# Kernel optimization log

Hardware: AMD Instinct MI355X
Metric: run time of the kernel (lower is better)

Reference implementation:

```python
import jax, jax.numpy as jnp
import numpy as np

B, N, C, H, K = 16, 1024, 384, 6, 8
HID = int(C * 2.0)  # mlp_ratio = 2.0
HD = C // H


def _layernorm(x, w, b, eps=1e-5):
    m = x.mean(-1, keepdims=True)
    v = ((x - m) ** 2).mean(-1, keepdims=True)
    return (x - m) * jax.lax.rsqrt(v + eps) * w + b


def setup_inputs() -> dict:
    key = jax.random.key(0)
    ks = jax.random.split(key, 16)
    x = jax.random.normal(ks[0], (B, N, C), jnp.float32)
    # knn indices within each batch, offset by batch*N (as in get_knn_index)
    idx = jax.random.randint(ks[1], (B, K, N), 0, N)
    base = jnp.arange(B, dtype=jnp.int32)[:, None, None] * N
    knn_index = (idx + base).reshape(-1).astype(jnp.int32)
    s = 0.02
    p = {
        "x": x,
        "knn_index": knn_index,
        "ln1_w": jnp.ones((C,), jnp.float32),
        "ln1_b": jnp.zeros((C,), jnp.float32),
        "w_qkv": jax.random.normal(ks[2], (C, 3 * C), jnp.float32) * s,  # qkv_bias=False
        "w_proj": jax.random.normal(ks[3], (C, C), jnp.float32) * s,
        "b_proj": jnp.zeros((C,), jnp.float32),
        "w_knn": jax.random.normal(ks[4], (2 * C, C), jnp.float32) * s,
        "b_knn": jnp.zeros((C,), jnp.float32),
        "w_merge": jax.random.normal(ks[5], (2 * C, C), jnp.float32) * s,
        "b_merge": jnp.zeros((C,), jnp.float32),
        "ln2_w": jnp.ones((C,), jnp.float32),
        "ln2_b": jnp.zeros((C,), jnp.float32),
        "w_fc1": jax.random.normal(ks[6], (C, HID), jnp.float32) * s,
        "b_fc1": jnp.zeros((HID,), jnp.float32),
        "w_fc2": jax.random.normal(ks[7], (HID, C), jnp.float32) * s,
        "b_fc2": jnp.zeros((C,), jnp.float32),
    }
    return p


def reference(x, knn_index, ln1_w, ln1_b, w_qkv, w_proj, b_proj, w_knn, b_knn,
              w_merge, b_merge, ln2_w, ln2_b, w_fc1, b_fc1, w_fc2, b_fc2):
    nx = _layernorm(x, ln1_w, ln1_b)  # [B,N,C]

    # --- self attention ---
    qkv = (nx @ w_qkv).reshape(B, N, 3, H, HD)
    q, k, v = qkv[:, :, 0], qkv[:, :, 1], qkv[:, :, 2]  # [B,N,H,HD]
    scale = HD ** (-0.5)
    attn = jnp.einsum("bnhd,bmhd->bhnm", q, k) * scale
    attn = jax.nn.softmax(attn, axis=-1)
    a_out = jnp.einsum("bhnm,bmhd->bnhd", attn, v).reshape(B, N, C)
    x1 = a_out @ w_proj + b_proj

    # --- graph feature: gather, relative concat, Linear+LeakyReLU, max over k ---
    feat = nx.reshape(B * N, C)[knn_index].reshape(B, K, N, C)
    center = nx[:, None, :, :]  # [B,1,N,C]
    g = jnp.concatenate([feat - center, jnp.broadcast_to(center, (B, K, N, C))], axis=-1)
    knn_f = jax.nn.leaky_relu(g @ w_knn + b_knn, negative_slope=0.2)
    knn_f = knn_f.max(axis=1)  # [B,N,C]

    x1 = jnp.concatenate([x1, knn_f], axis=-1) @ w_merge + b_merge
    x = x + x1

    # --- MLP ---
    h = _layernorm(x, ln2_w, ln2_b)
    h = jax.nn.gelu(h @ w_fc1 + b_fc1, approximate=False) @ w_fc2 + b_fc2
    return x + h
```

## Files before the change

### kernel.cpp

```cpp
#include <hip/hip_runtime.h>
#include <hip/hip_bf16.h>
#include <math.h>

#define BN_ROWS 16384
#define CDIM 384
#define NH 6
#define BBATCH 16
#define NNN 1024

typedef unsigned short u16;
typedef unsigned int u32;
typedef __attribute__((ext_vector_type(8))) short short8;
typedef __attribute__((ext_vector_type(4))) float floatx4;

__device__ __forceinline__ float b2f(u16 s) { return __uint_as_float(((u32)s) << 16); }
__device__ __forceinline__ u16 f2b(float f) {
    __hip_bfloat16 h = __float2bfloat16(f);
    u16 s; __builtin_memcpy(&s, &h, 2); return s;
}
__device__ __forceinline__ u32 cvt_pk_bf16(float lo, float hi) {
    u32 r;
    asm("v_cvt_pk_bf16_f32 %0, %1, %2" : "=v"(r) : "v"(lo), "v"(hi));
    return r;
}
__device__ __forceinline__ void gload_lds16(const u16* g, u16* l) {
    __builtin_amdgcn_global_load_lds(
        (const __attribute__((address_space(1))) unsigned int*)g,
        (__attribute__((address_space(3))) unsigned int*)l, 16, 0, 0);
}

__global__ __launch_bounds__(256) void pack_all(
    const float* __restrict__ W0, u16* __restrict__ T0,
    const float* __restrict__ W1, u16* __restrict__ T1,
    const float* __restrict__ W2, u16* __restrict__ T2,
    const float* __restrict__ W3, u16* __restrict__ T3,
    const float* __restrict__ W4, u16* __restrict__ T4,
    const float* __restrict__ W5, u16* __restrict__ T5)
{
    const float* W; u16* T; int K, N;
    switch (blockIdx.z) {
        case 0: W = W0; T = T0; K = 384; N = 1152; break;
        case 1: W = W1; T = T1; K = 384; N = 384;  break;
        case 2: W = W2; T = T2; K = 768; N = 384;  break;
        case 3: W = W3; T = T3; K = 768; N = 384;  break;
        case 4: W = W4; T = T4; K = 384; N = 768;  break;
        default: W = W5; T = T5; K = 768; N = 384; break;
    }
    const int n0 = blockIdx.x * 32, k0 = blockIdx.y * 32;
    if (n0 >= N || k0 >= K) return;
    __shared__ float s[32][33];
    const int tx = threadIdx.x & 31, ty = threadIdx.x >> 5;
#pragma unroll
    for (int i = 0; i < 4; ++i)
        s[ty + 8 * i][tx] = W[(size_t)(k0 + ty + 8 * i) * N + n0 + tx];
    __syncthreads();
#pragma unroll
    for (int i = 0; i < 4; ++i)
        T[(size_t)(n0 + ty + 8 * i) * K + k0 + tx] = f2b(s[tx][ty + 8 * i]);
}

__global__ __launch_bounds__(64) void ln_kernel(const float* __restrict__ xin,
                                                const float* __restrict__ w,
                                                const float* __restrict__ b,
                                                u16* __restrict__ out)
{
    const int row = blockIdx.x;
    const int t = threadIdx.x;
    const size_t base = (size_t)row * CDIM;
    float v[6];
#pragma unroll
    for (int i = 0; i < 6; ++i) v[i] = xin[base + t + 64 * i];
    float s = 0.f, s2 = 0.f;
#pragma unroll
    for (int i = 0; i < 6; ++i) { s += v[i]; s2 += v[i] * v[i]; }
#pragma unroll
    for (int m = 1; m < 64; m <<= 1) {
        s  += __shfl_xor(s,  m, 64);
        s2 += __shfl_xor(s2, m, 64);
    }
    const float mean = s * (1.0f / CDIM);
    const float var  = s2 * (1.0f / CDIM) - mean * mean;
    const float rs   = rsqrtf(var + 1e-5f);
#pragma unroll
    for (int i = 0; i < 6; ++i) {
        int c = t + 64 * i;
        out[base + c] = f2b((v[i] - mean) * rs * w[c] + b[c]);
    }
}

template<int ACT, bool HAS_BIAS, bool HAS_RES, bool OUT_F32, int MODE, int NT, bool SWZ>
__global__ __launch_bounds__(256) void gemm_mfma_kernel(
    const u16* __restrict__ A, int lda,
    const u16* __restrict__ Bt, const u16* __restrict__ Bt2, int ldbt,
    u16* Cb, u16* Cb2, float* Cf, int ldc,
    const float* __restrict__ bias,
    const float* res,
    int K)
{
    constexpr int NTL = NT / 32;
    __shared__ u16 As[2][128 * 32];
    __shared__ u16 Bs[2][NT * 32];
    const int tid  = threadIdx.x;
    const int wv   = tid >> 6;
    const int lane = tid & 63;
    const int l15  = lane & 15;
    const int quad = lane >> 4;

    int m0, n0;
    if (SWZ) {
        const int nbx = gridDim.x;
        const int total = nbx * gridDim.y;
        int lin = blockIdx.x + nbx * blockIdx.y;
        const int cpx = total >> 3;
        lin = (lin & 7) * cpx + (lin >> 3);
        m0 = (lin / nbx) * 128;
        n0 = (lin % nbx) * NT;
    } else {
        m0 = blockIdx.y * 128;
        n0 = blockIdx.x * NT;
    }

    const int woffm = (wv >> 1) * 64;
    const int woffn = (wv & 1) * (NT / 2);

    const u16* bsrc = (MODE == 2 && n0 >= 384) ? Bt2 : Bt;
    const int  bn0  = (MODE == 2 && n0 >= 384) ? (n0 - 384) : n0;

    floatx4 acc[4][NTL];
#pragma unroll
    for (int mt = 0; mt < 4; ++mt)
#pragma unroll
        for (int nt = 0; nt < NTL; ++nt) acc[mt][nt] = (floatx4){0.f, 0.f, 0.f, 0.f};

    const int gsw  = 8 * ((lane & 3) ^ ((lane >> 3) & 3));
    const int rloc = lane >> 2;
    const int rdsw = 8 * (quad ^ ((l15 >> 1) & 3));

    auto stage = [&](int kt, int p) {
#pragma unroll
        for (int j = 0; j < 2; ++j) {
            const int slab = 32 * wv + 16 * j;
            gload_lds16(A + (size_t)(m0 + slab + rloc) * lda + kt + gsw, &As[p][slab * 32]);
        }
        if (NT == 128) {
#pragma unroll
            for (int j = 0; j < 2; ++j) {
                const int slab = 32 * wv + 16 * j;
                gload_lds16(bsrc + (size_t)(bn0 + slab + rloc) * ldbt + kt + gsw, &Bs[p][slab * 32]);
            }
        } else {
            const int slab = 16 * wv;
            gload_lds16(bsrc + (size_t)(bn0 + slab + rloc) * ldbt + kt + gsw, &Bs[p][slab * 32]);
        }
    };

    stage(0, 0);
    stage(32, 1);
    int cur = 0;
    for (int kt = 0; kt < K; kt += 32) {
        if (kt + 32 < K) {
            if constexpr (NT == 128) asm volatile("s_waitcnt vmcnt(4)" ::: "memory");
            else                     asm volatile("s_waitcnt vmcnt(3)" ::: "memory");
        } else {
            asm volatile("s_waitcnt vmcnt(0)" ::: "memory");
        }
        __builtin_amdgcn_sched_barrier(0);
        __builtin_amdgcn_s_barrier();
        __builtin_amdgcn_sched_barrier(0);

        short8 af[4], bf[NTL];
#pragma unroll
        for (int mt = 0; mt < 4; ++mt)
            af[mt] = *(const short8*)(As[cur] + (woffm + mt * 16 + l15) * 32 + rdsw);
#pragma unroll
        for (int nt = 0; nt < NTL; ++nt)
            bf[nt] = *(const short8*)(Bs[cur] + (woffn + nt * 16 + l15) * 32 + rdsw);
#pragma unroll
        for (int mt = 0; mt < 4; ++mt)
#pragma unroll
            for (int nt = 0; nt < NTL; ++nt)
                acc[mt][nt] = __builtin_amdgcn_mfma_f32_16x16x32_bf16(
                    bf[nt], af[mt], acc[mt][nt], 0, 0, 0);
        __builtin_amdgcn_sched_barrier(0);
        __builtin_amdgcn_s_barrier();
        __builtin_amdgcn_sched_barrier(0);
        if (kt + 64 < K) stage(kt + 64, cur);
        cur ^= 1;
    }

#pragma unroll
    for (int mt = 0; mt < 4; ++mt) {
        const int gr = m0 + woffm + mt * 16 + l15;
#pragma unroll
        for (int nt = 0; nt < NTL; ++nt) {
            const int gc0 = n0 + woffn + nt * 16 + quad * 4;
            float v4[4];
#pragma unroll
            for (int rr = 0; rr < 4; ++rr) v4[rr] = acc[mt][nt][rr];
            if (HAS_BIAS) {
                const floatx4 bv = *(const floatx4*)(bias + gc0);
#pragma unroll
                for (int rr = 0; rr < 4; ++rr) v4[rr] += bv[rr];
            }
            if (MODE == 2) {
                if (gc0 >= 384) {
                    const floatx4 bv = *(const floatx4*)(bias + gc0 - 384);
#pragma unroll
                    for (int rr = 0; rr < 4; ++rr) v4[rr] += bv[rr];
                }
            }
            if (ACT == 1) {
#pragma unroll
                for (int rr = 0; rr < 4; ++rr)
                    v4[rr] = 0.5f * v4[rr] * (1.0f + erff(v4[rr] * 0.70710678118654752f));
            }
            if (HAS_RES) {
                const floatx4 rv = *(const floatx4*)(res + (size_t)gr * ldc + gc0);
#pragma unroll
                for (int rr = 0; rr < 4; ++rr) v4[rr] += rv[rr];
            }
            if (MODE == 1) {
                const int t3  = gc0 / 384;
                const int rem = gc0 - t3 * 384;
                const int hh = rem >> 6, dd = rem & 63;
                const int bb = gr >> 10, nn = gr & 1023;
                u32 lo = cvt_pk_bf16(v4[0], v4[1]);
                u32 hi = cvt_pk_bf16(v4[2], v4[3]);
                *(uint2*)(Cb + ((size_t)((bb * 6 + hh) * 1024 + nn)) * 192 + t3 * 64 + dd) =
                    make_uint2(lo, hi);
            } else if (MODE == 2) {
                u32 lo = cvt_pk_bf16(v4[0], v4[1]);
                u32 hi = cvt_pk_bf16(v4[2], v4[3]);
                if (gc0 < 384)
                    *(uint2*)(Cb  + (size_t)gr * 384 + gc0)       = make_uint2(lo, hi);
                else
                    *(uint2*)(Cb2 + (size_t)gr * 384 + gc0 - 384) = make_uint2(lo, hi);
            } else if (OUT_F32) {
                floatx4 vv = {v4[0], v4[1], v4[2], v4[3]};
                *(floatx4*)(Cf + (size_t)gr * ldc + gc0) = vv;
            } else {
                u32 lo = cvt_pk_bf16(v4[0], v4[1]);
                u32 hi = cvt_pk_bf16(v4[2], v4[3]);
                *(uint2*)(Cb + (size_t)gr * ldc + gc0) = make_uint2(lo, hi);
            }
        }
    }
}

__global__ __launch_bounds__(256) void attn_mfma_kernel(const u16* __restrict__ qkv2,
                                                        u16* __restrict__ aout)
{
    const int id = blockIdx.x;
    const int rxcd = id & 7;
    const int j = id >> 3;
    const int slab = rxcd + 8 * (j % 12);
    const int qtile = j / 12;
    const int b = slab / NH, h = slab % NH;

    const int wave = threadIdx.x >> 6;
    const int lane = threadIdx.x & 63;
    const int l15 = lane & 15;
    const int quad = lane >> 4;
    const int qbase = qtile * 128 + wave * 32;
    const int tid = threadIdx.x;

    const u16* slabp = qkv2 + ((size_t)(b * NH + h) << 10) * 192;

    __shared__ __align__(16) u16 Ks[64 * 72];
    __shared__ __align__(16) u16 Vt[64 * 72];
    __shared__ __align__(16) u16 Ps[4][32 * 72];
    __shared__ __align__(16) float Ls[4][32];

    short8 qf[2][2];
#pragma unroll
    for (int nt = 0; nt < 2; ++nt) {
        const u16* qrow = slabp + (size_t)(qbase + nt * 16 + l15) * 192;
        qf[nt][0] = *(const short8*)(qrow + quad * 8);
        qf[nt][1] = *(const short8*)(qrow + 32 + quad * 8);
    }

    float rowsum[2] = {0.f, 0.f};
    floatx4 Oacc[2][4];
#pragma unroll
    for (int mt = 0; mt < 2; ++mt)
#pragma unroll
        for (int nt = 0; nt < 4; ++nt) Oacc[mt][nt] = (floatx4){0.f, 0.f, 0.f, 0.f};

    const int key = tid >> 2, dblk = (tid & 3) * 16;
    const int kp2 = tid & 31, db = (tid >> 5) * 8;
    uint4 kr0, kr1, vr0, vr1;
    {
        const u16* kp = slabp + (size_t)key * 192 + 64 + dblk;
        kr0 = *(const uint4*)(kp);
        kr1 = *(const uint4*)(kp + 8);
        const u16* vp = slabp + (size_t)(2 * kp2) * 192 + 128 + db;
        vr0 = *(const uint4*)(vp);
        vr1 = *(const uint4*)(vp + 192);
    }

    for (int kc = 0; kc < NNN; kc += 64) {
        *(uint4*)(Ks + key * 72 + dblk)     = kr0;
        *(uint4*)(Ks + key * 72 + dblk + 8) = kr1;
        {
            u32 a0[4] = {vr0.x, vr0.y, vr0.z, vr0.w};
            u32 a1[4] = {vr1.x, vr1.y, vr1.z, vr1.w};
#pragma unroll
            for (int i = 0; i < 4; ++i) {
                u32 lo = __builtin_amdgcn_perm(a1[i], a0[i], 0x05040100u);
                u32 hi = __builtin_amdgcn_perm(a1[i], a0[i], 0x07060302u);
                *(u32*)(Vt + (size_t)(db + 2 * i)     * 72 + 2 * kp2) = lo;
                *(u32*)(Vt + (size_t)(db + 2 * i + 1) * 72 + 2 * kp2) = hi;
            }
        }
        __syncthreads();

        if (kc + 64 < NNN) {
            const u16* kp = slabp + (size_t)(kc + 64 + key) * 192 + 64 + dblk;
            kr0 = *(const uint4*)(kp);
            kr1 = *(const uint4*)(kp + 8);
            const u16* vp = slabp + (size_t)(kc + 64 + 2 * kp2) * 192 + 128 + db;
            vr0 = *(const uint4*)(vp);
            vr1 = *(const uint4*)(vp + 192);
        }

        floatx4 sc[4][2];
        __builtin_amdgcn_s_setprio(1);
#pragma unroll
        for (int kt_ = 0; kt_ < 4; ++kt_) {
            short8 kf0 = *(const short8*)(Ks + (kt_ * 16 + l15) * 72 + quad * 8);
            short8 kf1 = *(const short8*)(Ks + (kt_ * 16 + l15) * 72 + 32 + quad * 8);
#pragma unroll
            for (int nt = 0; nt < 2; ++nt) {
                floatx4 s = {0.f, 0.f, 0.f, 0.f};
                s = __builtin_amdgcn_mfma_f32_16x16x32_bf16(kf0, qf[nt][0], s, 0, 0, 0);
                s = __builtin_amdgcn_mfma_f32_16x16x32_bf16(kf1, qf[nt][1], s, 0, 0, 0);
                sc[kt_][nt] = s;
            }
        }
        __builtin_amdgcn_s_setprio(0);

#pragma unroll
        for (int kt_ = 0; kt_ < 4; ++kt_)
#pragma unroll
            for (int nt = 0; nt < 2; ++nt) {
                float pv[4];
#pragma unroll
                for (int rr = 0; rr < 4; ++rr) {
                    pv[rr] = __expf(sc[kt_][nt][rr] * 0.125f);
                    rowsum[nt] += pv[rr];
                }
                u32 lo = cvt_pk_bf16(pv[0], pv[1]);
                u32 hi = cvt_pk_bf16(pv[2], pv[3]);
                *(uint2*)(Ps[wave] + (nt * 16 + l15) * 72 + kt_ * 16 + quad * 4) =
                    make_uint2(lo, hi);
            }

        short8 pf[2][2];
#pragma unroll
        for (int mt = 0; mt < 2; ++mt) {
            pf[mt][0] = *(const short8*)(Ps[wave] + (mt * 16 + l15) * 72 + quad * 8);
            pf[mt][1] = *(const short8*)(Ps[wave] + (mt * 16 + l15) * 72 + 32 + quad * 8);
        }
        __builtin_amdgcn_s_setprio(1);
#pragma unroll
        for (int nt = 0; nt < 4; ++nt) {
#pragma unroll
            for (int kk = 0; kk < 2; ++kk) {
                short8 vf = *(const short8*)(Vt + (size_t)(nt * 16 + l15) * 72 + kk * 32 + quad * 8);
#pragma unroll
                for (int mt = 0; mt < 2; ++mt)
                    Oacc[mt][nt] = __builtin_amdgcn_mfma_f32_16x16x32_bf16(
                        pf[mt][kk], vf, Oacc[mt][nt], 0, 0, 0);
            }
        }
        __builtin_amdgcn_s_setprio(0);
        __syncthreads();
    }

#pragma unroll
    for (int nt = 0; nt < 2; ++nt) {
        float l = rowsum[nt];
        l += __shfl_xor(l, 16, 64);
        l += __shfl_xor(l, 32, 64);
        if (quad == 0) Ls[wave][nt * 16 + l15] = l;
    }
#pragma unroll
    for (int mt = 0; mt < 2; ++mt) {
        float4 lv = *(const float4*)&Ls[wave][mt * 16 + quad * 4];
        float li[4] = {lv.x, lv.y, lv.z, lv.w};
#pragma unroll
        for (int rr = 0; rr < 4; ++rr) {
            float inv = 1.0f / li[rr];
            int q = qbase + mt * 16 + quad * 4 + rr;
#pragma unroll
            for (int nt = 0; nt < 4; ++nt)
                aout[(size_t)(b * NNN + q) * CDIM + h * 64 + nt * 16 + l15] =
                    f2b(Oacc[mt][nt][rr] * inv);
        }
    }
}

__global__ __launch_bounds__(128) void knnmax_kernel(const u16* __restrict__ t1,
                                                     const u16* __restrict__ t2,
                                                     const int* __restrict__ idx,
                                                     u16* __restrict__ x1cat)
{
    const int bn = blockIdx.x * 2 + (threadIdx.x >> 6);
    const int lane = threadIdx.x & 63;
    if (lane >= 48) return;
    const int b = bn >> 10, n = bn & 1023;
    int ind[8];
#pragma unroll
    for (int k = 0; k < 8; ++k) ind[k] = idx[b * 8192 + k * 1024 + n];
    const int c0 = lane * 8;
    const size_t rbase = (size_t)bn * CDIM + c0;
    short8 v1 = *(const short8*)(t1 + rbase);
    short8 v2 = *(const short8*)(t2 + rbase);
    float basef[8], mx[8];
#pragma unroll
    for (int j = 0; j < 8; ++j) {
        basef[j] = b2f((u16)v2[j]) - b2f((u16)v1[j]);
        mx[j] = -1e30f;
    }
#pragma unroll
    for (int k = 0; k < 8; ++k) {
        short8 nv = *(const short8*)(t1 + (size_t)ind[k] * CDIM + c0);
#pragma unroll
        for (int j = 0; j < 8; ++j) {
            float v = b2f((u16)nv[j]) + basef[j];
            v = (v > 0.f) ? v : 0.2f * v;
            mx[j] = fmaxf(mx[j], v);
        }
    }
    short8 ov;
#pragma unroll
    for (int j = 0; j < 8; ++j) ov[j] = (short)f2b(mx[j]);
    *(short8*)(x1cat + (size_t)bn * 768 + CDIM + c0) = ov;
}

extern "C" void kernel_launch(void* const* d_in, const int* in_sizes, int n_in,
                              void* d_out, int out_size, void* d_ws, size_t ws_size,
                              hipStream_t stream)
{
    (void)in_sizes; (void)n_in; (void)out_size; (void)ws_size;
    const float* x     = (const float*)d_in[0];
    const int*   knn   = (const int*)d_in[1];
    const float* ln1w  = (const float*)d_in[2];
    const float* ln1b  = (const float*)d_in[3];
    const float* wqkv  = (const float*)d_in[4];
    const float* wproj = (const float*)d_in[5];
    const float* bproj = (const float*)d_in[6];
    const float* wknn  = (const float*)d_in[7];
    const float* bknn  = (const float*)d_in[8];
    const float* wmrg  = (const float*)d_in[9];
    const float* bmrg  = (const float*)d_in[10];
    const float* ln2w  = (const float*)d_in[11];
    const float* ln2b  = (const float*)d_in[12];
    const float* wfc1  = (const float*)d_in[13];
    const float* bfc1  = (const float*)d_in[14];
    const float* wfc2  = (const float*)d_in[15];
    const float* bfc2  = (const float*)d_in[16];

    u16* wsb = (u16*)d_ws;
    const size_t RE = (size_t)BN_ROWS * CDIM;
    u16* nxb   = wsb;
    u16* qkvb  = wsb + RE;
    u16* x1cat = wsb + RE;
    u16* t1b   = wsb + 3 * RE;
    u16* hinb  = wsb;
    u16* h1b   = wsb + RE;
    u16* wqkvT  = wsb + 4 * RE;
    u16* wprojT = wqkvT + 442368;
    u16* wknnT  = wprojT + 147456;
    u16* wmrgT  = wknnT + 294912;
    u16* wfc1T  = wmrgT + 294912;
    u16* wfc2T  = wfc1T + 294912;
    u16*   aoutb = (u16*)d_out;
    u16*   t2b   = (u16*)d_out;
    float* xmid  = (float*)d_out;

    pack_all<<<dim3(36, 24, 6), 256, 0, stream>>>(
        wqkv, wqkvT, wproj, wprojT, wknn, wknnT, wmrg, wmrgT, wfc1, wfc1T, wfc2, wfc2T);
    ln_kernel<<<BN_ROWS, 64, 0, stream>>>(x, ln1w, ln1b, nxb);
    gemm_mfma_kernel<0, false, false, false, 1, 128, true><<<dim3(9, 128), 256, 0, stream>>>(
        nxb, CDIM, wqkvT, nullptr, CDIM, qkvb, nullptr, nullptr, 0, nullptr, nullptr, CDIM);
    attn_mfma_kernel<<<768, 256, 0, stream>>>(qkvb, aoutb);
    gemm_mfma_kernel<0, true, false, false, 0, 64, true><<<dim3(6, 128), 256, 0, stream>>>(
        aoutb, CDIM, wprojT, nullptr, CDIM, x1cat, nullptr, nullptr, 768, bproj, nullptr, CDIM);
    gemm_mfma_kernel<0, false, false, false, 2, 128, true><<<dim3(6, 128), 256, 0, stream>>>(
        nxb, CDIM, wknnT, wknnT + 384, 768, t1b, t2b, nullptr, CDIM, bknn, nullptr, CDIM);
    knnmax_kernel<<<BN_ROWS / 2, 128, 0, stream>>>(t1b, t2b, knn, x1cat);
    gemm_mfma_kernel<0, true, true, true, 0, 64, true><<<dim3(6, 128), 256, 0, stream>>>(
        x1cat, 768, wmrgT, nullptr, 768, nullptr, nullptr, xmid, CDIM, bmrg, x, 768);
    ln_kernel<<<BN_ROWS, 64, 0, stream>>>(xmid, ln2w, ln2b, hinb);
    gemm_mfma_kernel<1, true, false, false, 0, 128, true><<<dim3(6, 128), 256, 0, stream>>>(
        hinb, CDIM, wfc1T, nullptr, CDIM, h1b, nullptr, nullptr, 768, bfc1, nullptr, CDIM);
    gemm_mfma_kernel<0, true, true, true, 0, 64, true><<<dim3(6, 128), 256, 0, stream>>>(
        h1b, 768, wfc2T, nullptr, 768, nullptr, nullptr, (float*)d_out, CDIM, bfc2, xmid, 768);
}
```

Baseline: 309.2 us.

## Shrink GEMM tiles to 64x64 with simpler double-buffered pipeline

```diff
diff --git a/kernel.cpp b/kernel.cpp
--- a/kernel.cpp
+++ b/kernel.cpp
@@ -88,8 +88,8 @@
     }
 }
 
-template<int ACT, bool HAS_BIAS, bool HAS_RES, bool OUT_F32, int MODE, int NT, bool SWZ>
-__global__ __launch_bounds__(256) void gemm_mfma_kernel(
+template<int ACT, bool HAS_BIAS, bool HAS_RES, bool OUT_F32, int MODE, bool SWZ>
+__global__ __launch_bounds__(256, 6) void gemm_mfma_kernel(
     const u16* __restrict__ A, int lda,
     const u16* __restrict__ Bt, const u16* __restrict__ Bt2, int ldbt,
     u16* Cb, u16* Cb2, float* Cf, int ldc,
@@ -97,9 +97,8 @@
     const float* res,
     int K)
 {
-    constexpr int NTL = NT / 32;
-    __shared__ u16 As[2][128 * 32];
-    __shared__ u16 Bs[2][NT * 32];
+    __shared__ u16 As[2][64 * 32];
+    __shared__ u16 Bs[2][64 * 32];
     const int tid  = threadIdx.x;
     const int wv   = tid >> 6;
     const int lane = tid & 63;
@@ -113,86 +112,63 @@
         int lin = blockIdx.x + nbx * blockIdx.y;
         const int cpx = total >> 3;
         lin = (lin & 7) * cpx + (lin >> 3);
-        m0 = (lin / nbx) * 128;
-        n0 = (lin % nbx) * NT;
+        m0 = (lin / nbx) * 64;
+        n0 = (lin % nbx) * 64;
     } else {
-        m0 = blockIdx.y * 128;
-        n0 = blockIdx.x * NT;
-    }
-
-    const int woffm = (wv >> 1) * 64;
-    const int woffn = (wv & 1) * (NT / 2);
+        m0 = blockIdx.y * 64;
+        n0 = blockIdx.x * 64;
+    }
+
+    const int woffm = (wv >> 1) * 32;
+    const int woffn = (wv & 1) * 32;
 
     const u16* bsrc = (MODE == 2 && n0 >= 384) ? Bt2 : Bt;
     const int  bn0  = (MODE == 2 && n0 >= 384) ? (n0 - 384) : n0;
 
-    floatx4 acc[4][NTL];
-#pragma unroll
-    for (int mt = 0; mt < 4; ++mt)
-#pragma unroll
-        for (int nt = 0; nt < NTL; ++nt) acc[mt][nt] = (floatx4){0.f, 0.f, 0.f, 0.f};
+    floatx4 acc[2][2];
+#pragma unroll
+    for (int mt = 0; mt < 2; ++mt)
+#pragma unroll
+        for (int nt = 0; nt < 2; ++nt) acc[mt][nt] = (floatx4){0.f, 0.f, 0.f, 0.f};
 
     const int gsw  = 8 * ((lane & 3) ^ ((lane >> 3) & 3));
     const int rloc = lane >> 2;
     const int rdsw = 8 * (quad ^ ((l15 >> 1) & 3));
 
     auto stage = [&](int kt, int p) {
-#pragma unroll
-        for (int j = 0; j < 2; ++j) {
-            const int slab = 32 * wv + 16 * j;
-            gload_lds16(A + (size_t)(m0 + slab + rloc) * lda + kt + gsw, &As[p][slab * 32]);
-        }
-        if (NT == 128) {
-#pragma unroll
-            for (int j = 0; j < 2; ++j) {
-                const int slab = 32 * wv + 16 * j;
-                gload_lds16(bsrc + (size_t)(bn0 + slab + rloc) * ldbt + kt + gsw, &Bs[p][slab * 32]);
-            }
-        } else {
-            const int slab = 16 * wv;
-            gload_lds16(bsrc + (size_t)(bn0 + slab + rloc) * ldbt + kt + gsw, &Bs[p][slab * 32]);
-        }
+        const int slab = 16 * wv;
+        gload_lds16(A    + (size_t)(m0  + slab + rloc) * lda  + kt + gsw, &As[p][slab * 32]);
+        gload_lds16(bsrc + (size_t)(bn0 + slab + rloc) * ldbt + kt + gsw, &Bs[p][slab * 32]);
     };
 
     stage(0, 0);
-    stage(32, 1);
+    __syncthreads();
     int cur = 0;
     for (int kt = 0; kt < K; kt += 32) {
-        if (kt + 32 < K) {
-            if constexpr (NT == 128) asm volatile("s_waitcnt vmcnt(4)" ::: "memory");
-            else                     asm volatile("s_waitcnt vmcnt(3)" ::: "memory");
-        } else {
-            asm volatile("s_waitcnt vmcnt(0)" ::: "memory");
-        }
-        __builtin_amdgcn_sched_barrier(0);
-        __builtin_amdgcn_s_barrier();
-        __builtin_amdgcn_sched_barrier(0);
-
-        short8 af[4], bf[NTL];
-#pragma unroll
-        for (int mt = 0; mt < 4; ++mt)
+        if (kt + 32 < K) stage(kt + 32, cur ^ 1);
+
+        short8 af[2], bf[2];
+#pragma unroll
+        for (int mt = 0; mt < 2; ++mt)
             af[mt] = *(const short8*)(As[cur] + (woffm + mt * 16 + l15) * 32 + rdsw);
 #pragma unroll
-        for (int nt = 0; nt < NTL; ++nt)
+        for (int nt = 0; nt < 2; ++nt)
             bf[nt] = *(const short8*)(Bs[cur] + (woffn + nt * 16 + l15) * 32 + rdsw);
 #pragma unroll
-        for (int mt = 0; mt < 4; ++mt)
-#pragma unroll
-            for (int nt = 0; nt < NTL; ++nt)
+        for (int mt = 0; mt < 2; ++mt)
+#pragma unroll
+            for (int nt = 0; nt < 2; ++nt)
                 acc[mt][nt] = __builtin_amdgcn_mfma_f32_16x16x32_bf16(
                     bf[nt], af[mt], acc[mt][nt], 0, 0, 0);
-        __builtin_amdgcn_sched_barrier(0);
-        __builtin_amdgcn_s_barrier();
-        __builtin_amdgcn_sched_barrier(0);
-        if (kt + 64 < K) stage(kt + 64, cur);
+        __syncthreads();
         cur ^= 1;
     }
 
 #pragma unroll
-    for (int mt = 0; mt < 4; ++mt) {
+    for (int mt = 0; mt < 2; ++mt) {
         const int gr = m0 + woffm + mt * 16 + l15;
 #pragma unroll
-        for (int nt = 0; nt < NTL; ++nt) {
+        for (int nt = 0; nt < 2; ++nt) {
             const int gc0 = n0 + woffn + nt * 16 + quad * 4;
             float v4[4];
 #pragma unroll
@@ -482,19 +458,19 @@
     pack_all<<<dim3(36, 24, 6), 256, 0, stream>>>(
         wqkv, wqkvT, wproj, wprojT, wknn, wknnT, wmrg, wmrgT, wfc1, wfc1T, wfc2, wfc2T);
     ln_kernel<<<BN_ROWS, 64, 0, stream>>>(x, ln1w, ln1b, nxb);
-    gemm_mfma_kernel<0, false, false, false, 1, 128, true><<<dim3(9, 128), 256, 0, stream>>>(
+    gemm_mfma_kernel<0, false, false, false, 1, true><<<dim3(18, 256), 256, 0, stream>>>(
         nxb, CDIM, wqkvT, nullptr, CDIM, qkvb, nullptr, nullptr, 0, nullptr, nullptr, CDIM);
     attn_mfma_kernel<<<768, 256, 0, stream>>>(qkvb, aoutb);
-    gemm_mfma_kernel<0, true, false, false, 0, 64, true><<<dim3(6, 128), 256, 0, stream>>>(
+    gemm_mfma_kernel<0, true, false, false, 0, true><<<dim3(6, 256), 256, 0, stream>>>(
         aoutb, CDIM, wprojT, nullptr, CDIM, x1cat, nullptr, nullptr, 768, bproj, nullptr, CDIM);
-    gemm_mfma_kernel<0, false, false, false, 2, 128, true><<<dim3(6, 128), 256, 0, stream>>>(
+    gemm_mfma_kernel<0, false, false, false, 2, true><<<dim3(12, 256), 256, 0, stream>>>(
         nxb, CDIM, wknnT, wknnT + 384, 768, t1b, t2b, nullptr, CDIM, bknn, nullptr, CDIM);
     knnmax_kernel<<<BN_ROWS / 2, 128, 0, stream>>>(t1b, t2b, knn, x1cat);
-    gemm_mfma_kernel<0, true, true, true, 0, 64, true><<<dim3(6, 128), 256, 0, stream>>>(
+    gemm_mfma_kernel<0, true, true, true, 0, true><<<dim3(6, 256), 256, 0, stream>>>(
         x1cat, 768, wmrgT, nullptr, 768, nullptr, nullptr, xmid, CDIM, bmrg, x, 768);
     ln_kernel<<<BN_ROWS, 64, 0, stream>>>(xmid, ln2w, ln2b, hinb);
-    gemm_mfma_kernel<1, true, false, false, 0, 128, true><<<dim3(6, 128), 256, 0, stream>>>(
+    gemm_mfma_kernel<1, true, false, false, 0, true><<<dim3(12, 256), 256, 0, stream>>>(
         hinb, CDIM, wfc1T, nullptr, CDIM, h1b, nullptr, nullptr, 768, bfc1, nullptr, CDIM);
-    gemm_mfma_kernel<0, true, true, true, 0, 64, true><<<dim3(6, 128), 256, 0, stream>>>(
+    gemm_mfma_kernel<0, true, true, true, 0, true><<<dim3(6, 256), 256, 0, stream>>>(
         h1b, 768, wfc2T, nullptr, 768, nullptr, nullptr, (float*)d_out, CDIM, bfc2, xmid, 768);
 }
```

Result: slower. 345.9 us (+11.9%).
